# Kernel tuning notes

Hardware: AMD Instinct MI355X
Metric: run time of the kernel (lower is better)

The kernel has to match this reference:

```python
import jax, jax.numpy as jnp
import numpy as np

EPS = 1e-5
D = 32          # token embedding dim
HEADS = 8
DH = D // HEADS  # 4


def _layernorm(x, g, b):
    mu = jnp.mean(x, axis=-1, keepdims=True)
    var = jnp.mean(jnp.square(x - mu), axis=-1, keepdims=True)
    return (x - mu) / jnp.sqrt(var + EPS) * g + b


def _mhsa(x, Wqvk, W0):
    # x: [..., t, 32]; Wqvk: [96, 32]; W0: [32, 32]
    qkv = x @ Wqvk.T                                   # [..., t, 96]
    qkv = qkv.reshape(qkv.shape[:-1] + (DH, 3, HEADS))  # (d k h) layout of original rearrange
    q, k, v = qkv[..., 0, :], qkv[..., 1, :], qkv[..., 2, :]  # [..., t, d, h]
    scores = jnp.einsum('...tdh,...sdh->...hts', q, k) * (DH ** -0.5)
    attn = jax.nn.softmax(scores, axis=-1)
    out = jnp.einsum('...hts,...sdh->...thd', attn, v)  # [..., t, h, d]
    out = out.reshape(out.shape[:-2] + (D,))            # (h d) concat order
    return out @ W0.T


def setup_inputs() -> dict:
    key = jax.random.key(0)
    ks = jax.random.split(key, 8)
    B = 256
    s = D ** -0.5
    return {
        'x':       jax.random.normal(ks[0], (B, 3, 32, 32, 32), dtype=jnp.float32),
        'pos_y':   jax.random.normal(ks[1], (3, 32, 32), dtype=jnp.float32) * s,
        'Wqvk_y':  jax.random.normal(ks[2], (3, 3 * D, D), dtype=jnp.float32) * s,
        'W0_y':    jax.random.normal(ks[3], (3, D, D), dtype=jnp.float32) * s,
        'g_y':     jnp.ones((D,), dtype=jnp.float32),
        'b_y':     jnp.zeros((D,), dtype=jnp.float32),
        'Wqvk_x':  jax.random.normal(ks[4], (3, 3 * D, D), dtype=jnp.float32) * s,
        'W0_x':    jax.random.normal(ks[5], (3, D, D), dtype=jnp.float32) * s,
        'g_x':     jnp.ones((D,), dtype=jnp.float32),
        'b_x':     jnp.zeros((D,), dtype=jnp.float32),
    }


def reference(x, pos_y, Wqvk_y, W0_y, g_y, b_y, Wqvk_x, W0_x, g_x, b_x):
    # x: [b, 3, l, w, h] with l=w=h=32. Dropout layers are in eval mode (identity).
    tst = jnp.transpose(x, (0, 1, 4, 2, 3))               # [b, 3, i(=h), t(=l), d(=w)]
    # AbsPosEmb1D per RGB channel: in_ @ pos^T
    emb = jnp.einsum('bcitd,cjd->bcitj', tst, pos_y)      # [b, 3, 32, 32, 32]
    outs = []
    for c in range(3):  # distinct r/g/b weights
        o = _mhsa(emb[:, c], Wqvk_y[c], W0_y[c])
        outs.append(_layernorm(emb[:, c] + o, g_y, b_y))
    x_tmp = jnp.stack(outs, axis=1)                       # [b, 3, i, t, 32]
    x_tmp = jnp.transpose(x_tmp, (0, 1, 3, 4, 2))         # [b, 3, t, 32, i]
    x1 = jax.nn.sigmoid(x_tmp) * x                        # first gating

    # BUG in original second loop: it reuses the stale `emb_y` from the last
    # iteration of the first loop (channel b, i = width-1) for every (i, j).
    emb_last = emb[:, 2, -1]                              # [b, 32, 32]
    ys = []
    for c in range(3):
        o = _mhsa(emb_last, Wqvk_x[c], W0_x[c])
        ys.append(_layernorm(emb_last + o, g_x, b_x))
    tmp2 = jnp.stack(ys, axis=1)                          # [b, 3, t, 32]
    # y stacked over i (constant across i), then permuted to [b,3,32,i,32]
    y_perm = jnp.transpose(tmp2, (0, 1, 3, 2))[:, :, :, None, :]  # [b,3,32,1,32]
    return jax.nn.sigmoid(y_perm) * x1
```

## Files before the change

### kernel.cpp

```cpp
#include <hip/hip_runtime.h>
#include <hip/hip_bf16.h>


using bf16 = __hip_bfloat16;
typedef float v2f __attribute__((ext_vector_type(2)));

__device__ __forceinline__ v2f pk_fma(v2f acc, v2f a, v2f b) {
  asm("v_pk_fma_f32 %0, %1, %2, %0" : "+v"(acc) : "v"(a), "v"(b));
  return acc;
}

struct __align__(16) SMem {
  float psJ[32][36];
  float wcF[96][34];
  float w0s[32][36];
  float xs[32][36];
  float qS[32][34];
  float kT[32][36];
  float vT[32][36];
};

__global__ __launch_bounds__(256) void wc_kernel(
    const float* __restrict__ pos_y, const float* __restrict__ wqvk_y,
    const float* __restrict__ wqvk_x, float* __restrict__ wc)
{
  const int n = blockIdx.x;
  const int c = n % 3, xset = n / 3;
  const float* W = (xset ? wqvk_x : wqvk_y) + c * 3072;
  const float* P = pos_y + (xset ? 2 : c) * 1024;
  __shared__ float Ws[96][33];
  __shared__ float Ps[32][33];
  const int tid = threadIdx.x;
#pragma unroll
  for (int k = 0; k < 12; ++k) {
    const int e = tid * 12 + k;
    Ws[e >> 5][e & 31] = W[e];
  }
#pragma unroll
  for (int k = 0; k < 4; ++k) {
    const int e = tid * 4 + k;
    Ps[e >> 5][e & 31] = P[e];
  }
  __syncthreads();
  const int fg = tid >> 3, d0 = (tid & 7) * 4;
#pragma unroll
  for (int m = 0; m < 3; ++m) {
    const int f = fg + 32 * m;
    float s0 = 0.f, s1 = 0.f, s2 = 0.f, s3 = 0.f;
#pragma unroll
    for (int j = 0; j < 32; ++j) {
      const float w = Ws[f][j];
      s0 += w * Ps[j][d0];     s1 += w * Ps[j][d0 + 1];
      s2 += w * Ps[j][d0 + 2]; s3 += w * Ps[j][d0 + 3];
    }
    const float sc = ((f % 24) < 8) ? 0.72134752f : 1.0f;
    float* o = wc + (size_t)n * 3072 + f * 32 + d0;
    o[0] = s0 * sc; o[1] = s1 * sc; o[2] = s2 * sc; o[3] = s3 * sc;
  }
}

__device__ __forceinline__ void load_tables(
    SMem& sm, int tid, const float* __restrict__ xbc, int i,
    const float* __restrict__ pos, const float* __restrict__ wcg,
    const float* __restrict__ w0g,
    const float* __restrict__ g, const float* __restrict__ b)
{
  const int t = tid >> 3, dq = (tid & 7) * 4;
  float xv0 = xbc[(t * 32 + dq + 0) * 32 + i];
  float xv1 = xbc[(t * 32 + dq + 1) * 32 + i];
  float xv2 = xbc[(t * 32 + dq + 2) * 32 + i];
  float xv3 = xbc[(t * 32 + dq + 3) * 32 + i];
  *(float4*)&sm.xs[t][dq] = make_float4(xv0, xv1, xv2, xv3);
  {
    const int e = tid * 4;
    float4 p = *(const float4*)&pos[e];
    *(float4*)&sm.psJ[e >> 5][e & 31] = p;
    float4 w = *(const float4*)&w0g[e];
    *(float4*)&sm.w0s[e >> 5][e & 31] = w;
  }
  {
    float wf[12];
    *(float4*)&wf[0] = *(const float4*)&wcg[tid * 12];
    *(float4*)&wf[4] = *(const float4*)&wcg[tid * 12 + 4];
    *(float4*)&wf[8] = *(const float4*)&wcg[tid * 12 + 8];
#pragma unroll
    for (int k = 0; k < 6; ++k) {
      const int e = tid * 12 + 2 * k;
      *(v2f*)&sm.wcF[e >> 5][e & 31] = v2f{wf[2 * k], wf[2 * k + 1]};
    }
  }
  if (tid < 32) {
    sm.xs[tid][33] = g[tid] * 1.44269504f;
    sm.xs[tid][34] = b[tid] * 1.44269504f;
  }
}

__device__ __forceinline__ void mhsa_core(SMem& sm, int tid, float sig_out[2][2])
{
  const int g = tid >> 4, l = tid & 15;
  float eres[2][2];

  {
    v2f a00{0.f,0.f}, a01{0.f,0.f}, a10{0.f,0.f}, a11{0.f,0.f};
#pragma unroll
    for (int d4 = 0; d4 < 8; ++d4) {
      float4 x0 = *(const float4*)&sm.xs[g][4 * d4];
      float4 x1 = *(const float4*)&sm.xs[g + 16][4 * d4];
      float4 p0 = *(const float4*)&sm.psJ[l][4 * d4];
      float4 p1 = *(const float4*)&sm.psJ[l + 16][4 * d4];
      a00 = pk_fma(a00, v2f{x0.x, x0.y}, v2f{p0.x, p0.y});
      a00 = pk_fma(a00, v2f{x0.z, x0.w}, v2f{p0.z, p0.w});
      a01 = pk_fma(a01, v2f{x0.x, x0.y}, v2f{p1.x, p1.y});
      a01 = pk_fma(a01, v2f{x0.z, x0.w}, v2f{p1.z, p1.w});
      a10 = pk_fma(a10, v2f{x1.x, x1.y}, v2f{p0.x, p0.y});
      a10 = pk_fma(a10, v2f{x1.z, x1.w}, v2f{p0.z, p0.w});
      a11 = pk_fma(a11, v2f{x1.x, x1.y}, v2f{p1.x, p1.y});
      a11 = pk_fma(a11, v2f{x1.z, x1.w}, v2f{p1.z, p1.w});
    }
    eres[0][0] = a00[0] + a00[1]; eres[0][1] = a01[0] + a01[1];
    eres[1][0] = a10[0] + a10[1]; eres[1][1] = a11[0] + a11[1];
  }
  {
    const int tg = (tid >> 5) * 4, rg = tid & 31;
    float* sp[3]; int st[3];
#pragma unroll
    for (int m = 0; m < 3; ++m) {
      const int f = rg + 32 * m;
      const int dh = f / 24, r2 = f - 24 * dh;
      const int sel = r2 >> 3, cc = (r2 & 7) * 4 + dh;
      if (sel == 0)      { sp[m] = &sm.qS[0][0] + cc;      st[m] = 34; }
      else if (sel == 1) { sp[m] = &sm.kT[0][0] + cc * 36; st[m] = 1;  }
      else               { sp[m] = &sm.vT[0][0] + cc * 36; st[m] = 1;  }
    }
    v2f acc[3][4];
#pragma unroll
    for (int m = 0; m < 3; ++m)
#pragma unroll
      for (int k = 0; k < 4; ++k) acc[m][k] = v2f{0.f, 0.f};
#pragma unroll
    for (int d4 = 0; d4 < 8; ++d4) {
      float4 a0 = *(const float4*)&sm.xs[tg + 0][4 * d4];
      float4 a1 = *(const float4*)&sm.xs[tg + 1][4 * d4];
      float4 a2 = *(const float4*)&sm.xs[tg + 2][4 * d4];
      float4 a3 = *(const float4*)&sm.xs[tg + 3][4 * d4];
#pragma unroll
      for (int m = 0; m < 3; ++m) {
        v2f wlo = *(const v2f*)&sm.wcF[rg + 32 * m][4 * d4];
        v2f whi = *(const v2f*)&sm.wcF[rg + 32 * m][4 * d4 + 2];
        acc[m][0] = pk_fma(acc[m][0], v2f{a0.x, a0.y}, wlo);
        acc[m][0] = pk_fma(acc[m][0], v2f{a0.z, a0.w}, whi);
        acc[m][1] = pk_fma(acc[m][1], v2f{a1.x, a1.y}, wlo);
        acc[m][1] = pk_fma(acc[m][1], v2f{a1.z, a1.w}, whi);
        acc[m][2] = pk_fma(acc[m][2], v2f{a2.x, a2.y}, wlo);
        acc[m][2] = pk_fma(acc[m][2], v2f{a2.z, a2.w}, whi);
        acc[m][3] = pk_fma(acc[m][3], v2f{a3.x, a3.y}, wlo);
        acc[m][3] = pk_fma(acc[m][3], v2f{a3.z, a3.w}, whi);
      }
    }
#pragma unroll
    for (int m = 0; m < 3; ++m) {
      const float r0 = acc[m][0][0] + acc[m][0][1];
      const float r1 = acc[m][1][0] + acc[m][1][1];
      const float r2v = acc[m][2][0] + acc[m][2][1];
      const float r3 = acc[m][3][0] + acc[m][3][1];
      if (st[m] == 1) {
        *(float4*)(sp[m] + tg) = make_float4(r0, r1, r2v, r3);
      } else {
        sp[m][(tg + 0) * 34] = r0;
        sp[m][(tg + 1) * 34] = r1;
        sp[m][(tg + 2) * 34] = r2v;
        sp[m][(tg + 3) * 34] = r3;
      }
    }
  }
  __syncthreads();

  {
    const int h = tid >> 5, tt = tid & 31;
    v2f qa = *(const v2f*)&sm.qS[tt][4 * h];
    v2f qb = *(const v2f*)&sm.qS[tt][4 * h + 2];
    v2f q0 = v2f{qa[0], qa[0]}, q1 = v2f{qa[1], qa[1]};
    v2f q2 = v2f{qb[0], qb[0]}, q3 = v2f{qb[1], qb[1]};
    const float* kr0 = &sm.kT[4 * h + 0][0];
    const float* kr1 = &sm.kT[4 * h + 1][0];
    const float* kr2 = &sm.kT[4 * h + 2][0];
    const float* kr3 = &sm.kT[4 * h + 3][0];
    v2f sc2[16];
#pragma unroll
    for (int s4 = 0; s4 < 8; ++s4) {
      float4 k0 = *(const float4*)&kr0[4 * s4];
      float4 k1 = *(const float4*)&kr1[4 * s4];
      float4 k2 = *(const float4*)&kr2[4 * s4];
      float4 k3 = *(const float4*)&kr3[4 * s4];
      v2f ea = v2f{0.f, 0.f}, eb = v2f{0.f, 0.f};
      ea = pk_fma(ea, q0, v2f{k0.x, k0.y}); eb = pk_fma(eb, q0, v2f{k0.z, k0.w});
      ea = pk_fma(ea, q1, v2f{k1.x, k1.y}); eb = pk_fma(eb, q1, v2f{k1.z, k1.w});
      ea = pk_fma(ea, q2, v2f{k2.x, k2.y}); eb = pk_fma(eb, q2, v2f{k2.z, k2.w});
      ea = pk_fma(ea, q3, v2f{k3.x, k3.y}); eb = pk_fma(eb, q3, v2f{k3.z, k3.w});
      sc2[2 * s4] = ea; sc2[2 * s4 + 1] = eb;
    }
    v2f den = v2f{0.f, 0.f};
#pragma unroll
    for (int s2 = 0; s2 < 16; ++s2) {
      sc2[s2][0] = exp2f(sc2[s2][0]);
      sc2[s2][1] = exp2f(sc2[s2][1]);
      den += sc2[s2];
    }
    const float inv = __fdividef(1.0f, den[0] + den[1]);
    const float* vr0 = &sm.vT[4 * h + 0][0];
    const float* vr1 = &sm.vT[4 * h + 1][0];
    const float* vr2 = &sm.vT[4 * h + 2][0];
    const float* vr3 = &sm.vT[4 * h + 3][0];
    v2f o0 = v2f{0.f,0.f}, o1 = v2f{0.f,0.f}, o2 = v2f{0.f,0.f}, o3 = v2f{0.f,0.f};
#pragma unroll
    for (int s4 = 0; s4 < 8; ++s4) {
      v2f aa = sc2[2 * s4], ab = sc2[2 * s4 + 1];
      float4 v0 = *(const float4*)&vr0[4 * s4];
      float4 v1 = *(const float4*)&vr1[4 * s4];
      float4 v2v = *(const float4*)&vr2[4 * s4];
      float4 v3 = *(const float4*)&vr3[4 * s4];
      o0 = pk_fma(o0, aa, v2f{v0.x, v0.y});   o0 = pk_fma(o0, ab, v2f{v0.z, v0.w});
      o1 = pk_fma(o1, aa, v2f{v1.x, v1.y});   o1 = pk_fma(o1, ab, v2f{v1.z, v1.w});
      o2 = pk_fma(o2, aa, v2f{v2v.x, v2v.y}); o2 = pk_fma(o2, ab, v2f{v2v.z, v2v.w});
      o3 = pk_fma(o3, aa, v2f{v3.x, v3.y});   o3 = pk_fma(o3, ab, v2f{v3.z, v3.w});
    }
    float4 ao;
    ao.x = (o0[0] + o0[1]) * inv;  ao.y = (o1[0] + o1[1]) * inv;
    ao.z = (o2[0] + o2[1]) * inv;  ao.w = (o3[0] + o3[1]) * inv;
    *(float4*)&sm.psJ[tt][4 * h] = ao;
  }
  __syncthreads();

  {
    v2f a00{0.f,0.f}, a01{0.f,0.f}, a10{0.f,0.f}, a11{0.f,0.f};
#pragma unroll
    for (int f4 = 0; f4 < 8; ++f4) {
      float4 u0 = *(const float4*)&sm.psJ[g][4 * f4];
      float4 u1 = *(const float4*)&sm.psJ[g + 16][4 * f4];
      float4 w0 = *(const float4*)&sm.w0s[l][4 * f4];
      float4 w1 = *(const float4*)&sm.w0s[l + 16][4 * f4];
      a00 = pk_fma(a00, v2f{u0.x, u0.y}, v2f{w0.x, w0.y});
      a00 = pk_fma(a00, v2f{u0.z, u0.w}, v2f{w0.z, w0.w});
      a01 = pk_fma(a01, v2f{u0.x, u0.y}, v2f{w1.x, w1.y});
      a01 = pk_fma(a01, v2f{u0.z, u0.w}, v2f{w1.z, w1.w});
      a10 = pk_fma(a10, v2f{u1.x, u1.y}, v2f{w0.x, w0.y});
      a10 = pk_fma(a10, v2f{u1.z, u1.w}, v2f{w0.z, w0.w});
      a11 = pk_fma(a11, v2f{u1.x, u1.y}, v2f{w1.x, w1.y});
      a11 = pk_fma(a11, v2f{u1.z, u1.w}, v2f{w1.z, w1.w});
    }
    float rr[2][2];
    rr[0][0] = a00[0] + a00[1] + eres[0][0];
    rr[0][1] = a01[0] + a01[1] + eres[0][1];
    rr[1][0] = a10[0] + a10[1] + eres[1][0];
    rr[1][1] = a11[0] + a11[1] + eres[1][1];
    float s1a = rr[0][0] + rr[0][1], s1b = rr[1][0] + rr[1][1];
    float s2a = rr[0][0]*rr[0][0] + rr[0][1]*rr[0][1];
    float s2b = rr[1][0]*rr[1][0] + rr[1][1]*rr[1][1];
#pragma unroll
    for (int m = 1; m < 16; m <<= 1) {
      s1a += __shfl_xor(s1a, m, 64);
      s2a += __shfl_xor(s2a, m, 64);
      s1b += __shfl_xor(s1b, m, 64);
      s2b += __shfl_xor(s2b, m, 64);
    }
    const float mua = s1a * (1.0f / 32.0f), mub = s1b * (1.0f / 32.0f);
    const float ra = rsqrtf(s2a * (1.0f / 32.0f) - mua * mua + 1e-5f);
    const float rb = rsqrtf(s2b * (1.0f / 32.0f) - mub * mub + 1e-5f);
    const float g0 = sm.xs[l][33],      b0 = sm.xs[l][34];
    const float g1 = sm.xs[l + 16][33], b1 = sm.xs[l + 16][34];
    sig_out[0][0] = __fdividef(1.0f, 1.0f + exp2f(-((rr[0][0] - mua) * ra * g0 + b0)));
    sig_out[0][1] = __fdividef(1.0f, 1.0f + exp2f(-((rr[0][1] - mua) * ra * g1 + b1)));
    sig_out[1][0] = __fdividef(1.0f, 1.0f + exp2f(-((rr[1][0] - mub) * rb * g0 + b0)));
    sig_out[1][1] = __fdividef(1.0f, 1.0f + exp2f(-((rr[1][1] - mub) * rb * g1 + b1)));
  }
}

__global__ __launch_bounds__(256, 4) void phase1_kernel(
    const float* __restrict__ x, const float* __restrict__ pos_y,
    const float* __restrict__ wc, const float* __restrict__ w0_x,
    const float* __restrict__ g_x, const float* __restrict__ b_x,
    bf16* __restrict__ gates)
{
  __shared__ SMem sm;
  const int tid = threadIdx.x;
  const int n = blockIdx.x;
  const int c = n % 3, b = n / 3;
  const float* xbc = x + (size_t)(b * 3 + 2) * 32768;
  load_tables(sm, tid, xbc, 31, pos_y + 2 * 1024,
              wc + (size_t)(3 + c) * 3072, w0_x + c * 1024, g_x, b_x);
  __syncthreads();
  float sig[2][2];
  mhsa_core(sm, tid, sig);
  const int g = tid >> 4, l = tid & 15;
#pragma unroll
  for (int u = 0; u < 2; ++u)
#pragma unroll
    for (int v = 0; v < 2; ++v)
      gates[((c * 256 + b) * 32 + g + 16 * u) * 32 + l + 16 * v] =
          __float2bfloat16(sig[u][v]);
}

__global__ __launch_bounds__(256, 4) void phase2_kernel(
    const float* __restrict__ x, const float* __restrict__ pos_y,
    const float* __restrict__ wc, const float* __restrict__ w0_y,
    const float* __restrict__ g_y, const float* __restrict__ b_y,
    const bf16* __restrict__ gates, float* __restrict__ out)
{
  __shared__ SMem sm;
  const int tid = threadIdx.x;
  const int n = blockIdx.x;
  const int p = (n & 7) * 3072 + (n >> 3);
  const int i = p & 31, bc = p >> 5;
  const int c = bc % 3, b = bc / 3;
  const float* xbc = x + (size_t)bc * 32768;
  load_tables(sm, tid, xbc, i, pos_y + c * 1024,
              wc + (size_t)c * 3072, w0_y + c * 1024, g_y, b_y);
  if (tid < 32)
    sm.xs[tid][32] = __bfloat162float(gates[((c * 256 + b) * 32 + i) * 32 + tid]);
  __syncthreads();
  float sig[2][2];
  mhsa_core(sm, tid, sig);
  const int g = tid >> 4, l = tid & 15;
  float* ob = out + (size_t)bc * 32768 + i;
#pragma unroll
  for (int u = 0; u < 2; ++u) {
    const int r = g + 16 * u;
    const float sgv = sm.xs[r][32];
#pragma unroll
    for (int v = 0; v < 2; ++v) {
      const int cc = l + 16 * v;
      ob[(r * 32 + cc) * 32] = sgv * sig[u][v] * sm.xs[r][cc];
    }
  }
}

extern "C" void kernel_launch(void* const* d_in, const int* in_sizes, int n_in,
                              void* d_out, int out_size, void* d_ws, size_t ws_size,
                              hipStream_t stream) {
  const float* x      = (const float*)d_in[0];
  const float* pos_y  = (const float*)d_in[1];
  const float* wqvk_y = (const float*)d_in[2];
  const float* w0_y   = (const float*)d_in[3];
  const float* g_y    = (const float*)d_in[4];
  const float* b_y    = (const float*)d_in[5];
  const float* wqvk_x = (const float*)d_in[6];
  const float* w0_x   = (const float*)d_in[7];
  const float* g_x    = (const float*)d_in[8];
  const float* b_x    = (const float*)d_in[9];
  bf16*  gates = (bf16*)d_ws;
  float* wcbuf = (float*)((char*)d_ws + 1572864);

  hipLaunchKernelGGL(wc_kernel, dim3(6), dim3(256), 0, stream,
                     pos_y, wqvk_y, wqvk_x, wcbuf);
  hipLaunchKernelGGL(phase1_kernel, dim3(768), dim3(256), 0, stream,
                     x, pos_y, wcbuf, w0_x, g_x, b_x, gates);
  hipLaunchKernelGGL(phase2_kernel, dim3(24576), dim3(256), 0, stream,
                     x, pos_y, wcbuf, w0_y, g_y, b_y, gates, (float*)d_out);
}
```

Baseline: 451.7 us.

## Fuse embedding into QKV pass, split attention across lanes, use DPP reductions

The positional-embedding product is computed inside the same loop as the QKV projection, so the xs loads are shared between them. The embedding result is staged in a new esT buffer for the residual add. Attention now gives each thread 4 query rows and 8 keys, with the softmax denominator and the PV partial sums combined across 4 lanes via DPP. LayerNorm reductions use DPP adds instead of __shfl_xor. W0 is loaded into the wcF buffer after the barrier, which frees the dedicated w0s array. This trades more register pressure and a tighter LDS layout for fewer shared loads and fewer cross-lane instructions.

```diff
diff --git a/kernel.cpp b/kernel.cpp
--- a/kernel.cpp
+++ b/kernel.cpp
@@ -10,14 +10,20 @@
   return acc;
 }
 
+template <int CTRL>
+__device__ __forceinline__ float dpp_add(float x) {
+  return x + __int_as_float(
+      __builtin_amdgcn_mov_dpp(__float_as_int(x), CTRL, 0xF, 0xF, true));
+}
+
 struct __align__(16) SMem {
   float psJ[32][36];
-  float wcF[96][34];
-  float w0s[32][36];
-  float xs[32][36];
-  float qS[32][34];
+  float wcF[96][36];
+  float xs[32][32];
+  float qS[32][36];
   float kT[32][36];
   float vT[32][36];
+  float esT[32][34];
 };
 
 __global__ __launch_bounds__(256) void wc_kernel(
@@ -62,7 +68,6 @@
 __device__ __forceinline__ void load_tables(
     SMem& sm, int tid, const float* __restrict__ xbc, int i,
     const float* __restrict__ pos, const float* __restrict__ wcg,
-    const float* __restrict__ w0g,
     const float* __restrict__ g, const float* __restrict__ b)
 {
   const int t = tid >> 3, dq = (tid & 7) * 4;
@@ -75,8 +80,6 @@
     const int e = tid * 4;
     float4 p = *(const float4*)&pos[e];
     *(float4*)&sm.psJ[e >> 5][e & 31] = p;
-    float4 w = *(const float4*)&w0g[e];
-    *(float4*)&sm.w0s[e >> 5][e & 31] = w;
   }
   {
     float wf[12];
@@ -90,72 +93,66 @@
     }
   }
   if (tid < 32) {
-    sm.xs[tid][33] = g[tid] * 1.44269504f;
-    sm.xs[tid][34] = b[tid] * 1.44269504f;
-  }
-}
-
-__device__ __forceinline__ void mhsa_core(SMem& sm, int tid, float sig_out[2][2])
-{
-  const int g = tid >> 4, l = tid & 15;
-  float eres[2][2];
-
-  {
-    v2f a00{0.f,0.f}, a01{0.f,0.f}, a10{0.f,0.f}, a11{0.f,0.f};
-#pragma unroll
-    for (int d4 = 0; d4 < 8; ++d4) {
-      float4 x0 = *(const float4*)&sm.xs[g][4 * d4];
-      float4 x1 = *(const float4*)&sm.xs[g + 16][4 * d4];
-      float4 p0 = *(const float4*)&sm.psJ[l][4 * d4];
-      float4 p1 = *(const float4*)&sm.psJ[l + 16][4 * d4];
-      a00 = pk_fma(a00, v2f{x0.x, x0.y}, v2f{p0.x, p0.y});
-      a00 = pk_fma(a00, v2f{x0.z, x0.w}, v2f{p0.z, p0.w});
-      a01 = pk_fma(a01, v2f{x0.x, x0.y}, v2f{p1.x, p1.y});
-      a01 = pk_fma(a01, v2f{x0.z, x0.w}, v2f{p1.z, p1.w});
-      a10 = pk_fma(a10, v2f{x1.x, x1.y}, v2f{p0.x, p0.y});
-      a10 = pk_fma(a10, v2f{x1.z, x1.w}, v2f{p0.z, p0.w});
-      a11 = pk_fma(a11, v2f{x1.x, x1.y}, v2f{p1.x, p1.y});
-      a11 = pk_fma(a11, v2f{x1.z, x1.w}, v2f{p1.z, p1.w});
-    }
-    eres[0][0] = a00[0] + a00[1]; eres[0][1] = a01[0] + a01[1];
-    eres[1][0] = a10[0] + a10[1]; eres[1][1] = a11[0] + a11[1];
-  }
-  {
-    const int tg = (tid >> 5) * 4, rg = tid & 31;
+    sm.qS[tid][32] = g[tid] * 1.44269504f;
+    sm.qS[tid][33] = b[tid] * 1.44269504f;
+  }
+}
+
+__device__ __forceinline__ void mhsa_core(SMem& sm, int tid,
+                                          const float* __restrict__ w0g,
+                                          float sig_out[2][2])
+{
+  {
+    const int u = tid >> 5, j = tid & 31;
+    const int tR = 4 * u;
     float* sp[3]; int st[3];
 #pragma unroll
     for (int m = 0; m < 3; ++m) {
-      const int f = rg + 32 * m;
+      const int f = j + 32 * m;
       const int dh = f / 24, r2 = f - 24 * dh;
       const int sel = r2 >> 3, cc = (r2 & 7) * 4 + dh;
-      if (sel == 0)      { sp[m] = &sm.qS[0][0] + cc;      st[m] = 34; }
+      if (sel == 0)      { sp[m] = &sm.qS[0][0] + cc;      st[m] = 36; }
       else if (sel == 1) { sp[m] = &sm.kT[0][0] + cc * 36; st[m] = 1;  }
       else               { sp[m] = &sm.vT[0][0] + cc * 36; st[m] = 1;  }
     }
-    v2f acc[3][4];
+    v2f ea[4], acc[3][4];
+#pragma unroll
+    for (int k = 0; k < 4; ++k) ea[k] = v2f{0.f, 0.f};
 #pragma unroll
     for (int m = 0; m < 3; ++m)
 #pragma unroll
       for (int k = 0; k < 4; ++k) acc[m][k] = v2f{0.f, 0.f};
 #pragma unroll
     for (int d4 = 0; d4 < 8; ++d4) {
-      float4 a0 = *(const float4*)&sm.xs[tg + 0][4 * d4];
-      float4 a1 = *(const float4*)&sm.xs[tg + 1][4 * d4];
-      float4 a2 = *(const float4*)&sm.xs[tg + 2][4 * d4];
-      float4 a3 = *(const float4*)&sm.xs[tg + 3][4 * d4];
-#pragma unroll
-      for (int m = 0; m < 3; ++m) {
-        v2f wlo = *(const v2f*)&sm.wcF[rg + 32 * m][4 * d4];
-        v2f whi = *(const v2f*)&sm.wcF[rg + 32 * m][4 * d4 + 2];
-        acc[m][0] = pk_fma(acc[m][0], v2f{a0.x, a0.y}, wlo);
-        acc[m][0] = pk_fma(acc[m][0], v2f{a0.z, a0.w}, whi);
-        acc[m][1] = pk_fma(acc[m][1], v2f{a1.x, a1.y}, wlo);
-        acc[m][1] = pk_fma(acc[m][1], v2f{a1.z, a1.w}, whi);
-        acc[m][2] = pk_fma(acc[m][2], v2f{a2.x, a2.y}, wlo);
-        acc[m][2] = pk_fma(acc[m][2], v2f{a2.z, a2.w}, whi);
-        acc[m][3] = pk_fma(acc[m][3], v2f{a3.x, a3.y}, wlo);
-        acc[m][3] = pk_fma(acc[m][3], v2f{a3.z, a3.w}, whi);
-      }
+      float4 x0 = *(const float4*)&sm.xs[tR + 0][4 * d4];
+      float4 x1 = *(const float4*)&sm.xs[tR + 1][4 * d4];
+      float4 x2 = *(const float4*)&sm.xs[tR + 2][4 * d4];
+      float4 x3 = *(const float4*)&sm.xs[tR + 3][4 * d4];
+      float4 pj = *(const float4*)&sm.psJ[j][4 * d4];
+      float4 wa = *(const float4*)&sm.wcF[j][4 * d4];
+      float4 wb = *(const float4*)&sm.wcF[j + 32][4 * d4];
+      float4 wc4 = *(const float4*)&sm.wcF[j + 64][4 * d4];
+      v2f pl{pj.x, pj.y}, ph{pj.z, pj.w};
+      v2f xl[4] = {v2f{x0.x,x0.y}, v2f{x1.x,x1.y}, v2f{x2.x,x2.y}, v2f{x3.x,x3.y}};
+      v2f xh[4] = {v2f{x0.z,x0.w}, v2f{x1.z,x1.w}, v2f{x2.z,x2.w}, v2f{x3.z,x3.w}};
+      v2f wl[3] = {v2f{wa.x,wa.y}, v2f{wb.x,wb.y}, v2f{wc4.x,wc4.y}};
+      v2f wh[3] = {v2f{wa.z,wa.w}, v2f{wb.z,wb.w}, v2f{wc4.z,wc4.w}};
+#pragma unroll
+      for (int k = 0; k < 4; ++k) {
+        ea[k] = pk_fma(ea[k], xl[k], pl);
+        ea[k] = pk_fma(ea[k], xh[k], ph);
+#pragma unroll
+        for (int m = 0; m < 3; ++m) {
+          acc[m][k] = pk_fma(acc[m][k], xl[k], wl[m]);
+          acc[m][k] = pk_fma(acc[m][k], xh[k], wh[m]);
+        }
+      }
+    }
+    {
+      const float e0 = ea[0][0] + ea[0][1], e1 = ea[1][0] + ea[1][1];
+      const float e2 = ea[2][0] + ea[2][1], e3 = ea[3][0] + ea[3][1];
+      *(v2f*)&sm.esT[j][tR]     = v2f{e0, e1};
+      *(v2f*)&sm.esT[j][tR + 2] = v2f{e2, e3};
     }
 #pragma unroll
     for (int m = 0; m < 3; ++m) {
@@ -164,81 +161,119 @@
       const float r2v = acc[m][2][0] + acc[m][2][1];
       const float r3 = acc[m][3][0] + acc[m][3][1];
       if (st[m] == 1) {
-        *(float4*)(sp[m] + tg) = make_float4(r0, r1, r2v, r3);
+        *(float4*)(sp[m] + tR) = make_float4(r0, r1, r2v, r3);
       } else {
-        sp[m][(tg + 0) * 34] = r0;
-        sp[m][(tg + 1) * 34] = r1;
-        sp[m][(tg + 2) * 34] = r2v;
-        sp[m][(tg + 3) * 34] = r3;
-      }
-    }
-  }
-  __syncthreads();
-
-  {
-    const int h = tid >> 5, tt = tid & 31;
-    v2f qa = *(const v2f*)&sm.qS[tt][4 * h];
-    v2f qb = *(const v2f*)&sm.qS[tt][4 * h + 2];
-    v2f q0 = v2f{qa[0], qa[0]}, q1 = v2f{qa[1], qa[1]};
-    v2f q2 = v2f{qb[0], qb[0]}, q3 = v2f{qb[1], qb[1]};
-    const float* kr0 = &sm.kT[4 * h + 0][0];
-    const float* kr1 = &sm.kT[4 * h + 1][0];
-    const float* kr2 = &sm.kT[4 * h + 2][0];
-    const float* kr3 = &sm.kT[4 * h + 3][0];
-    v2f sc2[16];
-#pragma unroll
-    for (int s4 = 0; s4 < 8; ++s4) {
-      float4 k0 = *(const float4*)&kr0[4 * s4];
-      float4 k1 = *(const float4*)&kr1[4 * s4];
-      float4 k2 = *(const float4*)&kr2[4 * s4];
-      float4 k3 = *(const float4*)&kr3[4 * s4];
-      v2f ea = v2f{0.f, 0.f}, eb = v2f{0.f, 0.f};
-      ea = pk_fma(ea, q0, v2f{k0.x, k0.y}); eb = pk_fma(eb, q0, v2f{k0.z, k0.w});
-      ea = pk_fma(ea, q1, v2f{k1.x, k1.y}); eb = pk_fma(eb, q1, v2f{k1.z, k1.w});
-      ea = pk_fma(ea, q2, v2f{k2.x, k2.y}); eb = pk_fma(eb, q2, v2f{k2.z, k2.w});
-      ea = pk_fma(ea, q3, v2f{k3.x, k3.y}); eb = pk_fma(eb, q3, v2f{k3.z, k3.w});
-      sc2[2 * s4] = ea; sc2[2 * s4 + 1] = eb;
-    }
-    v2f den = v2f{0.f, 0.f};
-#pragma unroll
-    for (int s2 = 0; s2 < 16; ++s2) {
-      sc2[s2][0] = exp2f(sc2[s2][0]);
-      sc2[s2][1] = exp2f(sc2[s2][1]);
-      den += sc2[s2];
-    }
-    const float inv = __fdividef(1.0f, den[0] + den[1]);
-    const float* vr0 = &sm.vT[4 * h + 0][0];
-    const float* vr1 = &sm.vT[4 * h + 1][0];
-    const float* vr2 = &sm.vT[4 * h + 2][0];
-    const float* vr3 = &sm.vT[4 * h + 3][0];
-    v2f o0 = v2f{0.f,0.f}, o1 = v2f{0.f,0.f}, o2 = v2f{0.f,0.f}, o3 = v2f{0.f,0.f};
-#pragma unroll
-    for (int s4 = 0; s4 < 8; ++s4) {
-      v2f aa = sc2[2 * s4], ab = sc2[2 * s4 + 1];
-      float4 v0 = *(const float4*)&vr0[4 * s4];
-      float4 v1 = *(const float4*)&vr1[4 * s4];
-      float4 v2v = *(const float4*)&vr2[4 * s4];
-      float4 v3 = *(const float4*)&vr3[4 * s4];
-      o0 = pk_fma(o0, aa, v2f{v0.x, v0.y});   o0 = pk_fma(o0, ab, v2f{v0.z, v0.w});
-      o1 = pk_fma(o1, aa, v2f{v1.x, v1.y});   o1 = pk_fma(o1, ab, v2f{v1.z, v1.w});
-      o2 = pk_fma(o2, aa, v2f{v2v.x, v2v.y}); o2 = pk_fma(o2, ab, v2f{v2v.z, v2v.w});
-      o3 = pk_fma(o3, aa, v2f{v3.x, v3.y});   o3 = pk_fma(o3, ab, v2f{v3.z, v3.w});
-    }
-    float4 ao;
-    ao.x = (o0[0] + o0[1]) * inv;  ao.y = (o1[0] + o1[1]) * inv;
-    ao.z = (o2[0] + o2[1]) * inv;  ao.w = (o3[0] + o3[1]) * inv;
-    *(float4*)&sm.psJ[tt][4 * h] = ao;
-  }
-  __syncthreads();
-
-  {
+        sp[m][(tR + 0) * 36] = r0;
+        sp[m][(tR + 1) * 36] = r1;
+        sp[m][(tR + 2) * 36] = r2v;
+        sp[m][(tR + 3) * 36] = r3;
+      }
+    }
+  }
+  float4 w0v = *(const float4*)&w0g[tid * 4];
+  __syncthreads();
+  {
+    const int e = tid * 4;
+    *(float4*)&sm.wcF[e >> 5][e & 31] = w0v;
+  }
+
+  {
+    const int h = tid >> 5, tg2 = (tid >> 2) & 7, sg2 = tid & 3;
+    const int ta = 4 * tg2, s0 = 8 * sg2;
+    float4 qr0 = *(const float4*)&sm.qS[ta + 0][4 * h];
+    float4 qr1 = *(const float4*)&sm.qS[ta + 1][4 * h];
+    float4 qr2 = *(const float4*)&sm.qS[ta + 2][4 * h];
+    float4 qr3 = *(const float4*)&sm.qS[ta + 3][4 * h];
+    const float qa_[4][4] = {
+        {qr0.x, qr0.y, qr0.z, qr0.w},
+        {qr1.x, qr1.y, qr1.z, qr1.w},
+        {qr2.x, qr2.y, qr2.z, qr2.w},
+        {qr3.x, qr3.y, qr3.z, qr3.w}};
+    v2f sc[4][4];
+#pragma unroll
+    for (int kk = 0; kk < 4; ++kk)
+#pragma unroll
+      for (int sp2 = 0; sp2 < 4; ++sp2) sc[kk][sp2] = v2f{0.f, 0.f};
+#pragma unroll
+    for (int dh = 0; dh < 4; ++dh) {
+      const float* kr = &sm.kT[4 * h + dh][s0];
+      float4 ka = *(const float4*)&kr[0];
+      float4 kb = *(const float4*)&kr[4];
+      v2f k0{ka.x, ka.y}, k1{ka.z, ka.w}, k2{kb.x, kb.y}, k3{kb.z, kb.w};
+#pragma unroll
+      for (int kk = 0; kk < 4; ++kk) {
+        v2f qv{qa_[kk][dh], qa_[kk][dh]};
+        sc[kk][0] = pk_fma(sc[kk][0], qv, k0);
+        sc[kk][1] = pk_fma(sc[kk][1], qv, k1);
+        sc[kk][2] = pk_fma(sc[kk][2], qv, k2);
+        sc[kk][3] = pk_fma(sc[kk][3], qv, k3);
+      }
+    }
+    float inv[4];
+#pragma unroll
+    for (int kk = 0; kk < 4; ++kk) {
+#pragma unroll
+      for (int sp2 = 0; sp2 < 4; ++sp2) {
+        sc[kk][sp2][0] = exp2f(sc[kk][sp2][0]);
+        sc[kk][sp2][1] = exp2f(sc[kk][sp2][1]);
+      }
+      v2f dv = sc[kk][0] + sc[kk][1];
+      v2f dw = sc[kk][2] + sc[kk][3];
+      dv += dw;
+      float dn = dv[0] + dv[1];
+      dn = dpp_add<0xB1>(dn);
+      dn = dpp_add<0x4E>(dn);
+      inv[kk] = __fdividef(1.0f, dn);
+    }
+    v2f pv[4][4];
+#pragma unroll
+    for (int kk = 0; kk < 4; ++kk)
+#pragma unroll
+      for (int dh = 0; dh < 4; ++dh) pv[kk][dh] = v2f{0.f, 0.f};
+#pragma unroll
+    for (int dh = 0; dh < 4; ++dh) {
+      const float* vr = &sm.vT[4 * h + dh][s0];
+      float4 va = *(const float4*)&vr[0];
+      float4 vb = *(const float4*)&vr[4];
+      v2f v0{va.x, va.y}, v1{va.z, va.w}, v2v{vb.x, vb.y}, v3{vb.z, vb.w};
+#pragma unroll
+      for (int kk = 0; kk < 4; ++kk) {
+        pv[kk][dh] = pk_fma(pv[kk][dh], sc[kk][0], v0);
+        pv[kk][dh] = pk_fma(pv[kk][dh], sc[kk][1], v1);
+        pv[kk][dh] = pk_fma(pv[kk][dh], sc[kk][2], v2v);
+        pv[kk][dh] = pk_fma(pv[kk][dh], sc[kk][3], v3);
+      }
+    }
+    float ov[4][4];
+#pragma unroll
+    for (int kk = 0; kk < 4; ++kk)
+#pragma unroll
+      for (int dh = 0; dh < 4; ++dh) {
+        float o = pv[kk][dh][0] + pv[kk][dh][1];
+        o = dpp_add<0xB1>(o);
+        o = dpp_add<0x4E>(o);
+        ov[kk][dh] = o;
+      }
+    if (sg2 == 0) {
+#pragma unroll
+      for (int kk = 0; kk < 4; ++kk) {
+        *(float4*)&sm.psJ[ta + kk][4 * h] = make_float4(
+            ov[kk][0] * inv[kk], ov[kk][1] * inv[kk],
+            ov[kk][2] * inv[kk], ov[kk][3] * inv[kk]);
+      }
+    }
+  }
+  __syncthreads();
+
+  {
+    const int g = tid >> 4, l = tid & 15;
     v2f a00{0.f,0.f}, a01{0.f,0.f}, a10{0.f,0.f}, a11{0.f,0.f};
 #pragma unroll
     for (int f4 = 0; f4 < 8; ++f4) {
       float4 u0 = *(const float4*)&sm.psJ[g][4 * f4];
       float4 u1 = *(const float4*)&sm.psJ[g + 16][4 * f4];
-      float4 w0 = *(const float4*)&sm.w0s[l][4 * f4];
-      float4 w1 = *(const float4*)&sm.w0s[l + 16][4 * f4];
+      float4 w0 = *(const float4*)&sm.wcF[l][4 * f4];
+      float4 w1 = *(const float4*)&sm.wcF[l + 16][4 * f4];
       a00 = pk_fma(a00, v2f{u0.x, u0.y}, v2f{w0.x, w0.y});
       a00 = pk_fma(a00, v2f{u0.z, u0.w}, v2f{w0.z, w0.w});
       a01 = pk_fma(a01, v2f{u0.x, u0.y}, v2f{w1.x, w1.y});
@@ -249,25 +284,26 @@
       a11 = pk_fma(a11, v2f{u1.z, u1.w}, v2f{w1.z, w1.w});
     }
     float rr[2][2];
-    rr[0][0] = a00[0] + a00[1] + eres[0][0];
-    rr[0][1] = a01[0] + a01[1] + eres[0][1];
-    rr[1][0] = a10[0] + a10[1] + eres[1][0];
-    rr[1][1] = a11[0] + a11[1] + eres[1][1];
+    rr[0][0] = a00[0] + a00[1] + sm.esT[l][g];
+    rr[0][1] = a01[0] + a01[1] + sm.esT[l + 16][g];
+    rr[1][0] = a10[0] + a10[1] + sm.esT[l][g + 16];
+    rr[1][1] = a11[0] + a11[1] + sm.esT[l + 16][g + 16];
     float s1a = rr[0][0] + rr[0][1], s1b = rr[1][0] + rr[1][1];
     float s2a = rr[0][0]*rr[0][0] + rr[0][1]*rr[0][1];
     float s2b = rr[1][0]*rr[1][0] + rr[1][1]*rr[1][1];
-#pragma unroll
-    for (int m = 1; m < 16; m <<= 1) {
-      s1a += __shfl_xor(s1a, m, 64);
-      s2a += __shfl_xor(s2a, m, 64);
-      s1b += __shfl_xor(s1b, m, 64);
-      s2b += __shfl_xor(s2b, m, 64);
-    }
+    s1a = dpp_add<0xB1>(s1a); s1a = dpp_add<0x4E>(s1a);
+    s1a = dpp_add<0x124>(s1a); s1a = dpp_add<0x128>(s1a);
+    s2a = dpp_add<0xB1>(s2a); s2a = dpp_add<0x4E>(s2a);
+    s2a = dpp_add<0x124>(s2a); s2a = dpp_add<0x128>(s2a);
+    s1b = dpp_add<0xB1>(s1b); s1b = dpp_add<0x4E>(s1b);
+    s1b = dpp_add<0x124>(s1b); s1b = dpp_add<0x128>(s1b);
+    s2b = dpp_add<0xB1>(s2b); s2b = dpp_add<0x4E>(s2b);
+    s2b = dpp_add<0x124>(s2b); s2b = dpp_add<0x128>(s2b);
     const float mua = s1a * (1.0f / 32.0f), mub = s1b * (1.0f / 32.0f);
     const float ra = rsqrtf(s2a * (1.0f / 32.0f) - mua * mua + 1e-5f);
     const float rb = rsqrtf(s2b * (1.0f / 32.0f) - mub * mub + 1e-5f);
-    const float g0 = sm.xs[l][33],      b0 = sm.xs[l][34];
-    const float g1 = sm.xs[l + 16][33], b1 = sm.xs[l + 16][34];
+    const float g0 = sm.qS[l][32],      b0 = sm.qS[l][33];
+    const float g1 = sm.qS[l + 16][32], b1 = sm.qS[l + 16][33];
     sig_out[0][0] = __fdividef(1.0f, 1.0f + exp2f(-((rr[0][0] - mua) * ra * g0 + b0)));
     sig_out[0][1] = __fdividef(1.0f, 1.0f + exp2f(-((rr[0][1] - mua) * ra * g1 + b1)));
     sig_out[1][0] = __fdividef(1.0f, 1.0f + exp2f(-((rr[1][0] - mub) * rb * g0 + b0)));
@@ -287,10 +323,10 @@
   const int c = n % 3, b = n / 3;
   const float* xbc = x + (size_t)(b * 3 + 2) * 32768;
   load_tables(sm, tid, xbc, 31, pos_y + 2 * 1024,
-              wc + (size_t)(3 + c) * 3072, w0_x + c * 1024, g_x, b_x);
+              wc + (size_t)(3 + c) * 3072, g_x, b_x);
   __syncthreads();
   float sig[2][2];
-  mhsa_core(sm, tid, sig);
+  mhsa_core(sm, tid, w0_x + c * 1024, sig);
   const int g = tid >> 4, l = tid & 15;
 #pragma unroll
   for (int u = 0; u < 2; ++u)
@@ -314,18 +350,18 @@
   const int c = bc % 3, b = bc / 3;
   const float* xbc = x + (size_t)bc * 32768;
   load_tables(sm, tid, xbc, i, pos_y + c * 1024,
-              wc + (size_t)c * 3072, w0_y + c * 1024, g_y, b_y);
+              wc + (size_t)c * 3072, g_y, b_y);
   if (tid < 32)
-    sm.xs[tid][32] = __bfloat162float(gates[((c * 256 + b) * 32 + i) * 32 + tid]);
+    sm.kT[tid][32] = __bfloat162float(gates[((c * 256 + b) * 32 + i) * 32 + tid]);
   __syncthreads();
   float sig[2][2];
-  mhsa_core(sm, tid, sig);
+  mhsa_core(sm, tid, w0_y + c * 1024, sig);
   const int g = tid >> 4, l = tid & 15;
   float* ob = out + (size_t)bc * 32768 + i;
 #pragma unroll
   for (int u = 0; u < 2; ++u) {
     const int r = g + 16 * u;
-    const float sgv = sm.xs[r][32];
+    const float sgv = sm.kT[r][32];
 #pragma unroll
     for (int v = 0; v < 2; ++v) {
       const int cc = l + 16 * v;
```

Measured after the change: 446.1 us. Within noise of the previous version (-1.2%).
